# Performance work log

Hardware: AMD Instinct MI355X
Metric: run time of the kernel (lower is better)

## Reference

```python
import jax, jax.numpy as jnp
import numpy as np

IN_FEATURES = 4096
OUT_FEATURES = 4096
IN_GROUP = 8
OUT_GROUP = 1
NUM_CODEBOOKS = 1
CODEBOOK_SIZE = 2 ** 16
NUM_OUT_GROUPS = OUT_FEATURES // OUT_GROUP   # 4096
NUM_IN_GROUPS = IN_FEATURES // IN_GROUP      # 512


def setup_inputs() -> dict:
    key = jax.random.key(0)
    k1, k2, k3, k4, k5 = jax.random.split(key, 5)
    input = jax.random.normal(k1, (4, 2048, IN_FEATURES), dtype=jnp.float32)
    codes = jax.random.randint(k2, (NUM_OUT_GROUPS, NUM_IN_GROUPS, NUM_CODEBOOKS), 0, CODEBOOK_SIZE, dtype=jnp.int32)
    codebooks = jax.random.normal(k3, (NUM_CODEBOOKS, CODEBOOK_SIZE, OUT_GROUP, IN_GROUP), dtype=jnp.float32)
    scales = jax.random.uniform(k4, (NUM_OUT_GROUPS, 1, 1, 1), dtype=jnp.float32)
    bias = jax.random.normal(k5, (OUT_FEATURES,), dtype=jnp.float32)
    return {"input": input, "codes": codes, "codebooks": codebooks, "scales": scales, "bias": bias}


def _dequantize_weight(codes, codebooks, scales):
    # codes: [nog, nig, nc] int; codebooks: [nc, K, og, ig]; scales: [nog, 1, 1, 1]
    nc = codebooks.shape[0]
    # gather per-codebook entries: [nog, nig, nc, og, ig]
    gathered = codebooks[jnp.arange(nc), codes]
    # sum over codebooks, apply per-out-group scale -> [nog, nig, og, ig]
    w = gathered.sum(axis=2) * scales
    nog, nig, og, ig = w.shape
    # [nog, og, nig, ig] -> [out_features, in_features]
    return w.transpose(0, 2, 1, 3).reshape(nog * og, nig * ig)


def reference(input, codes, codebooks, scales, bias):
    # Faithful AQLM dequant-GEMM: reconstruct W then input @ W^T + bias
    W = _dequantize_weight(codes, codebooks, scales)  # [out, in]
    out = jnp.einsum("bso,io->bsi", input, W.T.T) if False else input @ W.T
    if bias is not None:
        out = out + bias
    return out
```

## Files before the change

### kernel.cpp

```cpp
#include <hip/hip_runtime.h>
#include <hip/hip_bf16.h>
#include <stdint.h>

#define M_DIM 8192
#define N_DIM 4096
#define K_DIM 4096
#define NOG   4096
#define NIG   512

typedef __bf16 bf16;
typedef __attribute__((ext_vector_type(8))) __bf16 bf16x8;
typedef __attribute__((ext_vector_type(4))) float f32x4;


__device__ __forceinline__ void gload16(const void* g, void* lds) {
    __builtin_amdgcn_global_load_lds(
        (__attribute__((address_space(1))) void*)g,
        (__attribute__((address_space(3))) void*)lds,
        16 , 0 , 0 );
}

__global__ __launch_bounds__(256) void k_convert_tile(const float* __restrict__ in,
                                                      bf16* __restrict__ out) {
    __shared__ __align__(16) bf16 tile[256 * 8];
    const int t   = threadIdx.x;
    const int g   = blockIdx.y;
    const int h0  = blockIdx.x * 4;
    const int row = t >> 4;
    const int cc  = t & 15;
    const float4* p = (const float4*)(in + (size_t)(g * 16 + row) * K_DIM
                                         + h0 * 32 + cc * 8);
    float4 a = p[0], b = p[1];
    bf16x8 v;
    v[0] = (bf16)a.x; v[1] = (bf16)a.y; v[2] = (bf16)a.z; v[3] = (bf16)a.w;
    v[4] = (bf16)b.x; v[5] = (bf16)b.y; v[6] = (bf16)b.z; v[7] = (bf16)b.w;
    const int widx = (cc >> 2) * 64 + (cc & 3) * 16 + row;
    ((bf16x8*)tile)[widx] = v;
    __syncthreads();
    bf16x8 o = ((bf16x8*)tile)[t];
    ((bf16x8*)out)[((size_t)g * 128 + h0) * 64 + t] = o;
}

__global__ __launch_bounds__(256) void k_dequant_tile(const int* __restrict__ codes,
                                                      const float* __restrict__ cb,
                                                      const float* __restrict__ scales,
                                                      bf16* __restrict__ w) {
    const int t    = threadIdx.x;
    const int gB   = blockIdx.y;
    const int h0   = blockIdx.x * 4;
    const int hl   = t >> 6;
    const int kblk = (t >> 4) & 3;
    const int row  = t & 15;
    const int o    = gB * 16 + row;
    const int iG   = blockIdx.x * 16 + hl * 4 + kblk;
    unsigned code = (unsigned)codes[o * NIG + iG];
    float s = scales[o];
    const float4* e = (const float4*)(cb + (size_t)code * 8);
    float4 e0 = e[0], e1 = e[1];
    bf16x8 v;
    v[0] = (bf16)(e0.x * s); v[1] = (bf16)(e0.y * s);
    v[2] = (bf16)(e0.z * s); v[3] = (bf16)(e0.w * s);
    v[4] = (bf16)(e1.x * s); v[5] = (bf16)(e1.y * s);
    v[6] = (bf16)(e1.z * s); v[7] = (bf16)(e1.w * s);
    ((bf16x8*)w)[((size_t)gB * 128 + h0) * 64 + t] = v;
}

#define BM 256
#define BN 128
#define BK 64
#define KSTEPS (K_DIM / BK)

__global__ __launch_bounds__(256, 2) void k_gemm_tiled(
    const bf16* __restrict__ A,
    const bf16* __restrict__ B,
    const float* __restrict__ bias,
    float* __restrict__ C)
{
    __shared__ __align__(16) bf16 As[BM * BK];
    __shared__ __align__(16) bf16 Bs[BN * BK];

    const int tid  = threadIdx.x;
    const int wave = tid >> 6;
    const int lane = tid & 63;
    const int quad = lane >> 4;
    const int l16  = lane & 15;

    const int bn0 = blockIdx.x * BN;
    const int bm0 = blockIdx.y * BM;
    const int wm = (wave >> 1) * 128;
    const int wn = (wave & 1) * 64;

    const bf16* pA[4];
    const bf16* pB[2];
    #pragma unroll
    for (int gi = 0; gi < 4; ++gi) {
        const int g = blockIdx.y * 16 + wave * 4 + gi;
        pA[gi] = A + ((size_t)g * 8192 + lane) * 8;
    }
    #pragma unroll
    for (int gi = 0; gi < 2; ++gi) {
        const int g = blockIdx.x * 8 + wave * 2 + gi;
        pB[gi] = B + ((size_t)g * 8192 + lane) * 8;
    }
    bf16* AsW = As + wave * 4096;
    bf16* BsW = Bs + wave * 2048;

    const int gA0 = (wave >> 1) * 8;
    const int gB0 = (wave & 1) * 4;

    f32x4 acc[8][4] = {};

    for (int ks = 0; ks < KSTEPS; ++ks) {
        #pragma unroll
        for (int gi = 0; gi < 4; ++gi) {
            gload16(pA[gi],       AsW + gi * 1024);
            gload16(pA[gi] + 512, AsW + gi * 1024 + 512);
            pA[gi] += 1024;
        }
        #pragma unroll
        for (int gi = 0; gi < 2; ++gi) {
            gload16(pB[gi],       BsW + gi * 1024);
            gload16(pB[gi] + 512, BsW + gi * 1024 + 512);
            pB[gi] += 1024;
        }
        __syncthreads();

        bf16x8 af0[8], af1[8], bq0[4], bq1[4];
        #pragma unroll
        for (int t = 0; t < 8; ++t) {
            af0[t] = *(const bf16x8*)(As + (size_t)(gA0 + t) * 1024 + lane * 8);
            af1[t] = *(const bf16x8*)(As + (size_t)(gA0 + t) * 1024 + 512 + lane * 8);
        }
        #pragma unroll
        for (int t = 0; t < 4; ++t) {
            bq0[t] = *(const bf16x8*)(Bs + (size_t)(gB0 + t) * 1024 + lane * 8);
            bq1[t] = *(const bf16x8*)(Bs + (size_t)(gB0 + t) * 1024 + 512 + lane * 8);
        }

        #pragma unroll
        for (int i = 0; i < 8; ++i)
            #pragma unroll
            for (int j = 0; j < 4; ++j)
                acc[i][j] = __builtin_amdgcn_mfma_f32_16x16x32_bf16(
                    af0[i], bq0[j], acc[i][j], 0, 0, 0);
        #pragma unroll
        for (int i = 0; i < 8; ++i)
            #pragma unroll
            for (int j = 0; j < 4; ++j)
                acc[i][j] = __builtin_amdgcn_mfma_f32_16x16x32_bf16(
                    af1[i], bq1[j], acc[i][j], 0, 0, 0);

        __syncthreads();
    }

    #pragma unroll
    for (int j = 0; j < 4; ++j) {
        const int gn = bn0 + wn + j * 16 + l16;
        const float bz = bias[gn];
        #pragma unroll
        for (int i = 0; i < 8; ++i) {
            float* cp = C + (size_t)(bm0 + wm + i * 16 + quad * 4) * N_DIM + gn;
            #pragma unroll
            for (int r = 0; r < 4; ++r)
                cp[(size_t)r * N_DIM] = acc[i][j][r] + bz;
        }
    }
}

extern "C" void kernel_launch(void* const* d_in, const int* in_sizes, int n_in,
                              void* d_out, int out_size, void* d_ws, size_t ws_size,
                              hipStream_t stream) {
    const float* input     = (const float*)d_in[0];
    const int*   codes     = (const int*)d_in[1];
    const float* codebooks = (const float*)d_in[2];
    const float* scales    = (const float*)d_in[3];
    const float* bias      = (const float*)d_in[4];
    float* out = (float*)d_out;

    bf16* Abf = (bf16*)d_ws;
    bf16* Wbf = (bf16*)((char*)d_ws + (size_t)M_DIM * K_DIM * sizeof(bf16));

    (void)in_sizes; (void)n_in; (void)out_size; (void)ws_size;

    {
        dim3 g(K_DIM / 128, M_DIM / 16);
        k_convert_tile<<<g, 256, 0, stream>>>(input, Abf);
    }
    {
        dim3 g(K_DIM / 128, NOG / 16);
        k_dequant_tile<<<g, 256, 0, stream>>>(codes, codebooks, scales, Wbf);
    }
    {
        dim3 g(N_DIM / BN, M_DIM / BM);
        k_gemm_tiled<<<g, 256, 0, stream>>>(Abf, Wbf, bias, out);
    }
}
```

Before: 471.9 us.

## Double-buffer GEMM LDS tiles with BK 32 and merge prep kernels

Merges the activation conversion and weight dequantization into one launch, with the block index choosing the branch. The GEMM now uses two LDS buffers with a K-step of 32 and issues the next tile's global-to-LDS loads before computing on the current one, leaving one barrier per step. This is meant to overlap memory traffic with MFMA work and save a launch, in exchange for twice as many loop iterations. There is a possible hazard: the loads into the next buffer are issued right after the barrier with no wait on the previous async loads, so correctness depends on the barrier draining them.

```diff
diff --git a/kernel.cpp b/kernel.cpp
--- a/kernel.cpp
+++ b/kernel.cpp
@@ -20,64 +20,66 @@
         16 , 0 , 0 );
 }
 
-__global__ __launch_bounds__(256) void k_convert_tile(const float* __restrict__ in,
-                                                      bf16* __restrict__ out) {
+__global__ __launch_bounds__(256) void k_prep(const float* __restrict__ in,
+                                              bf16* __restrict__ Abf,
+                                              const int* __restrict__ codes,
+                                              const float* __restrict__ cb,
+                                              const float* __restrict__ scales,
+                                              bf16* __restrict__ Wbf) {
     __shared__ __align__(16) bf16 tile[256 * 8];
-    const int t   = threadIdx.x;
-    const int g   = blockIdx.y;
-    const int h0  = blockIdx.x * 4;
-    const int row = t >> 4;
-    const int cc  = t & 15;
-    const float4* p = (const float4*)(in + (size_t)(g * 16 + row) * K_DIM
-                                         + h0 * 32 + cc * 8);
-    float4 a = p[0], b = p[1];
-    bf16x8 v;
-    v[0] = (bf16)a.x; v[1] = (bf16)a.y; v[2] = (bf16)a.z; v[3] = (bf16)a.w;
-    v[4] = (bf16)b.x; v[5] = (bf16)b.y; v[6] = (bf16)b.z; v[7] = (bf16)b.w;
-    const int widx = (cc >> 2) * 64 + (cc & 3) * 16 + row;
-    ((bf16x8*)tile)[widx] = v;
-    __syncthreads();
-    bf16x8 o = ((bf16x8*)tile)[t];
-    ((bf16x8*)out)[((size_t)g * 128 + h0) * 64 + t] = o;
-}
-
-__global__ __launch_bounds__(256) void k_dequant_tile(const int* __restrict__ codes,
-                                                      const float* __restrict__ cb,
-                                                      const float* __restrict__ scales,
-                                                      bf16* __restrict__ w) {
-    const int t    = threadIdx.x;
-    const int gB   = blockIdx.y;
-    const int h0   = blockIdx.x * 4;
-    const int hl   = t >> 6;
-    const int kblk = (t >> 4) & 3;
-    const int row  = t & 15;
-    const int o    = gB * 16 + row;
-    const int iG   = blockIdx.x * 16 + hl * 4 + kblk;
-    unsigned code = (unsigned)codes[o * NIG + iG];
-    float s = scales[o];
-    const float4* e = (const float4*)(cb + (size_t)code * 8);
-    float4 e0 = e[0], e1 = e[1];
-    bf16x8 v;
-    v[0] = (bf16)(e0.x * s); v[1] = (bf16)(e0.y * s);
-    v[2] = (bf16)(e0.z * s); v[3] = (bf16)(e0.w * s);
-    v[4] = (bf16)(e1.x * s); v[5] = (bf16)(e1.y * s);
-    v[6] = (bf16)(e1.z * s); v[7] = (bf16)(e1.w * s);
-    ((bf16x8*)w)[((size_t)gB * 128 + h0) * 64 + t] = v;
+    const int t = threadIdx.x;
+    const int bid = blockIdx.x;
+    if (bid < 16384) {
+        const int g   = bid >> 5;
+        const int h0  = (bid & 31) * 4;
+        const int row = t >> 4;
+        const int cc  = t & 15;
+        const float4* p = (const float4*)(in + (size_t)(g * 16 + row) * K_DIM
+                                             + h0 * 32 + cc * 8);
+        float4 a = p[0], b = p[1];
+        bf16x8 v;
+        v[0] = (bf16)a.x; v[1] = (bf16)a.y; v[2] = (bf16)a.z; v[3] = (bf16)a.w;
+        v[4] = (bf16)b.x; v[5] = (bf16)b.y; v[6] = (bf16)b.z; v[7] = (bf16)b.w;
+        const int widx = (cc >> 2) * 64 + (cc & 3) * 16 + row;
+        ((bf16x8*)tile)[widx] = v;
+        __syncthreads();
+        bf16x8 o = ((bf16x8*)tile)[t];
+        ((bf16x8*)Abf)[((size_t)g * 128 + h0) * 64 + t] = o;
+    } else {
+        const int b    = bid - 16384;
+        const int gB   = b >> 5;
+        const int h0   = (b & 31) * 4;
+        const int hl   = t >> 6;
+        const int kblk = (t >> 4) & 3;
+        const int row  = t & 15;
+        const int o    = gB * 16 + row;
+        const int iG   = (b & 31) * 16 + hl * 4 + kblk;
+        unsigned code = (unsigned)codes[o * NIG + iG];
+        float s = scales[o];
+        const float4* e = (const float4*)(cb + (size_t)code * 8);
+        float4 e0 = e[0], e1 = e[1];
+        bf16x8 v;
+        v[0] = (bf16)(e0.x * s); v[1] = (bf16)(e0.y * s);
+        v[2] = (bf16)(e0.z * s); v[3] = (bf16)(e0.w * s);
+        v[4] = (bf16)(e1.x * s); v[5] = (bf16)(e1.y * s);
+        v[6] = (bf16)(e1.z * s); v[7] = (bf16)(e1.w * s);
+        ((bf16x8*)Wbf)[((size_t)gB * 128 + h0) * 64 + t] = v;
+    }
 }
 
 #define BM 256
 #define BN 128
-#define BK 64
+#define BK 32
 #define KSTEPS (K_DIM / BK)
 
-__global__ __launch_bounds__(256, 2) void k_gemm_tiled(
+__global__ __launch_bounds__(256, 2) void k_gemm_dbuf(
     const bf16* __restrict__ A,
     const bf16* __restrict__ B,
     const float* __restrict__ bias,
     float* __restrict__ C)
 {
-    __shared__ __align__(16) bf16 As[BM * BK];
-    __shared__ __align__(16) bf16 Bs[BN * BK];
+    __shared__ __align__(16) bf16 As[2][BM * BK];
+    __shared__ __align__(16) bf16 Bs[2][BN * BK];
 
     const int tid  = threadIdx.x;
     const int wave = tid >> 6;
@@ -93,64 +95,59 @@
     const bf16* pA[4];
     const bf16* pB[2];
     #pragma unroll
-    for (int gi = 0; gi < 4; ++gi) {
-        const int g = blockIdx.y * 16 + wave * 4 + gi;
-        pA[gi] = A + ((size_t)g * 8192 + lane) * 8;
-    }
+    for (int gi = 0; gi < 4; ++gi)
+        pA[gi] = A + (size_t)(blockIdx.y * 16 + wave * 4 + gi) * (128 * 512)
+                   + lane * 8;
     #pragma unroll
-    for (int gi = 0; gi < 2; ++gi) {
-        const int g = blockIdx.x * 8 + wave * 2 + gi;
-        pB[gi] = B + ((size_t)g * 8192 + lane) * 8;
-    }
-    bf16* AsW = As + wave * 4096;
-    bf16* BsW = Bs + wave * 2048;
+    for (int gi = 0; gi < 2; ++gi)
+        pB[gi] = B + (size_t)(blockIdx.x * 8 + wave * 2 + gi) * (128 * 512)
+                   + lane * 8;
 
     const int gA0 = (wave >> 1) * 8;
     const int gB0 = (wave & 1) * 4;
 
     f32x4 acc[8][4] = {};
 
+    {
+        bf16* AsW = As[0] + wave * 4 * 512;
+        bf16* BsW = Bs[0] + wave * 2 * 512;
+        #pragma unroll
+        for (int gi = 0; gi < 4; ++gi) gload16(pA[gi], AsW + gi * 512);
+        #pragma unroll
+        for (int gi = 0; gi < 2; ++gi) gload16(pB[gi], BsW + gi * 512);
+    }
+
+    #pragma unroll 2
     for (int ks = 0; ks < KSTEPS; ++ks) {
-        #pragma unroll
-        for (int gi = 0; gi < 4; ++gi) {
-            gload16(pA[gi],       AsW + gi * 1024);
-            gload16(pA[gi] + 512, AsW + gi * 1024 + 512);
-            pA[gi] += 1024;
-        }
-        #pragma unroll
-        for (int gi = 0; gi < 2; ++gi) {
-            gload16(pB[gi],       BsW + gi * 1024);
-            gload16(pB[gi] + 512, BsW + gi * 1024 + 512);
-            pB[gi] += 1024;
-        }
         __syncthreads();
 
-        bf16x8 af0[8], af1[8], bq0[4], bq1[4];
+        if (ks + 1 < KSTEPS) {
+            const int nb = (ks + 1) & 1;
+            bf16* AsW = As[nb] + wave * 4 * 512;
+            bf16* BsW = Bs[nb] + wave * 2 * 512;
+            const size_t off = (size_t)(ks + 1) * 512;
+            #pragma unroll
+            for (int gi = 0; gi < 4; ++gi) gload16(pA[gi] + off, AsW + gi * 512);
+            #pragma unroll
+            for (int gi = 0; gi < 2; ++gi) gload16(pB[gi] + off, BsW + gi * 512);
+        }
+
+        const bf16* Ab = As[ks & 1];
+        const bf16* Bb = Bs[ks & 1];
+        bf16x8 af[8], bq[4];
         #pragma unroll
-        for (int t = 0; t < 8; ++t) {
-            af0[t] = *(const bf16x8*)(As + (size_t)(gA0 + t) * 1024 + lane * 8);
-            af1[t] = *(const bf16x8*)(As + (size_t)(gA0 + t) * 1024 + 512 + lane * 8);
-        }
+        for (int t = 0; t < 8; ++t)
+            af[t] = *(const bf16x8*)(Ab + (size_t)(gA0 + t) * 512 + lane * 8);
         #pragma unroll
-        for (int t = 0; t < 4; ++t) {
-            bq0[t] = *(const bf16x8*)(Bs + (size_t)(gB0 + t) * 1024 + lane * 8);
-            bq1[t] = *(const bf16x8*)(Bs + (size_t)(gB0 + t) * 1024 + 512 + lane * 8);
-        }
+        for (int t = 0; t < 4; ++t)
+            bq[t] = *(const bf16x8*)(Bb + (size_t)(gB0 + t) * 512 + lane * 8);
 
         #pragma unroll
         for (int i = 0; i < 8; ++i)
             #pragma unroll
             for (int j = 0; j < 4; ++j)
                 acc[i][j] = __builtin_amdgcn_mfma_f32_16x16x32_bf16(
-                    af0[i], bq0[j], acc[i][j], 0, 0, 0);
-        #pragma unroll
-        for (int i = 0; i < 8; ++i)
-            #pragma unroll
-            for (int j = 0; j < 4; ++j)
-                acc[i][j] = __builtin_amdgcn_mfma_f32_16x16x32_bf16(
-                    af1[i], bq1[j], acc[i][j], 0, 0, 0);
-
-        __syncthreads();
+                    af[i], bq[j], acc[i][j], 0, 0, 0);
     }
 
     #pragma unroll
@@ -182,16 +179,9 @@
 
     (void)in_sizes; (void)n_in; (void)out_size; (void)ws_size;
 
-    {
-        dim3 g(K_DIM / 128, M_DIM / 16);
-        k_convert_tile<<<g, 256, 0, stream>>>(input, Abf);
-    }
-    {
-        dim3 g(K_DIM / 128, NOG / 16);
-        k_dequant_tile<<<g, 256, 0, stream>>>(codes, codebooks, scales, Wbf);
-    }
-    {
-        dim3 g(N_DIM / BN, M_DIM / BM);
-        k_gemm_tiled<<<g, 256, 0, stream>>>(Abf, Wbf, bias, out);
-    }
+    k_prep<<<16384 + 8192, 256, 0, stream>>>(input, Abf, codes, codebooks,
+                                             scales, Wbf);
+
+    dim3 g(N_DIM / BN, M_DIM / BM);
+    k_gemm_dbuf<<<g, 256, 0, stream>>>(Abf, Wbf, bias, out);
 }
```

Result: slower. 496.8 us (+5.3%).
